# Optimization experiments

Hardware: AMD Instinct MI355X
Metric: run time of the kernel (lower is better)

Reference implementation:

```python
import jax, jax.numpy as jnp
import numpy as np
from jax.scipy.linalg import expm

B, S, D, E, K, NROT = 2, 2048, 1024, 8, 2, 3
EPS = 1e-5


def setup_inputs() -> dict:
    key = jax.random.key(0)
    ks = jax.random.split(key, 16)
    sc = 0.02
    x = jax.random.normal(ks[0], (B, S, D), jnp.float32)
    ln_gamma = 1.0 + sc * jax.random.normal(ks[1], (D,), jnp.float32)
    ln_beta = sc * jax.random.normal(ks[2], (D,), jnp.float32)
    abel_w = sc * jax.random.normal(ks[3], (D, D), jnp.float32)
    abel_b = sc * jax.random.normal(ks[4], (D,), jnp.float32)
    moe_gate_w = sc * jax.random.normal(ks[5], (D, E), jnp.float32)
    moe_gate_b = sc * jax.random.normal(ks[6], (E,), jnp.float32)
    ew1 = sc * jax.random.normal(ks[7], (E, D, 2 * D), jnp.float32)
    eb1 = sc * jax.random.normal(ks[8], (E, 2 * D), jnp.float32)
    ew2 = sc * jax.random.normal(ks[9], (E, 2 * D, D), jnp.float32)
    eb2 = sc * jax.random.normal(ks[10], (E, D), jnp.float32)
    g = sc * jax.random.normal(ks[11], (NROT, D, D), jnp.float32)
    gens = 0.5 * (g - jnp.swapaxes(g, -1, -2))  # skew-symmetric, as in reset_parameters
    gc_w = sc * jax.random.normal(ks[12], (2 * D, 1), jnp.float32)
    gc_b = sc * jax.random.normal(ks[13], (1,), jnp.float32)
    return dict(x=x, ln_gamma=ln_gamma, ln_beta=ln_beta, abel_w=abel_w, abel_b=abel_b,
                moe_gate_w=moe_gate_w, moe_gate_b=moe_gate_b, ew1=ew1, eb1=eb1,
                ew2=ew2, eb2=eb2, gens=gens, gc_w=gc_w, gc_b=gc_b)


def _gelu(x):
    return jax.nn.gelu(x, approximate=False)  # torch nn.GELU default = exact erf


def _forward(x, ln_gamma, ln_beta, abel_w, abel_b, moe_gate_w, moe_gate_b,
             ew1, eb1, ew2, eb2, gens, gc_w, gc_b):
    residual = x
    # LayerNorm
    mu = jnp.mean(x, axis=-1, keepdims=True)
    var = jnp.mean((x - mu) ** 2, axis=-1, keepdims=True)
    xn = (x - mu) * jax.lax.rsqrt(var + EPS) * ln_gamma + ln_beta
    # abel branch: Linear + GELU
    abel_out = _gelu(xn @ abel_w + abel_b)
    # MoE: dense all-experts compute, masked by top-k softmax weights
    logits = xn @ moe_gate_w + moe_gate_b                      # [B,S,E]
    topw, topi = jax.lax.top_k(logits, K)                      # [B,S,K]
    topw = jax.nn.softmax(topw, axis=-1)
    w_dense = jnp.sum(jax.nn.one_hot(topi, E, dtype=xn.dtype) * topw[..., None], axis=-2)  # [B,S,E]
    h = _gelu(jnp.einsum('bsd,edh->ebsh', xn, ew1) + eb1[:, None, None, :])  # [E,B,S,2D]
    eo = jnp.einsum('ebsh,ehd->ebsd', h, ew2) + eb2[:, None, None, :]        # [E,B,S,D]
    moe_out = jnp.einsum('ebsd,bse->bsd', eo, w_dense)
    # GeometricRotation: sequential matrix_exp rotations
    for i in range(NROT):
        moe_out = moe_out @ expm(gens[i])
    # gated residual mix
    combined = jnp.concatenate([abel_out, moe_out], axis=-1)
    gate = jax.nn.sigmoid(combined @ gc_w + gc_b)              # [B,S,1]
    mixed = abel_out * (1.0 - gate) + moe_out * gate
    return residual + mixed


def reference(x, ln_gamma, ln_beta, abel_w, abel_b, moe_gate_w, moe_gate_b,
              ew1, eb1, ew2, eb2, gens, gc_w, gc_b):
    return _forward(x, ln_gamma, ln_beta, abel_w, abel_b, moe_gate_w, moe_gate_b,
                    ew1, eb1, ew2, eb2, gens, gc_w, gc_b)
```

## Files before the change

### kernel.cpp

```cpp
#include <hip/hip_runtime.h>
#include <hip/hip_bf16.h>
#include <cstdint>
#include <cstddef>

#define DD   1024
#define DD2  2048
#define EE   8
#define NTOK 4096
#define CAPR 10240

typedef __bf16 bf16_t;
typedef __bf16 bf16x8 __attribute__((ext_vector_type(8)));
typedef __bf16 bf16x4 __attribute__((ext_vector_type(4)));
typedef float  f32x4v __attribute__((ext_vector_type(4)));

__device__ __forceinline__ float gelu_f(float v){
  const float t = v*(0.7978845608028654f + 0.0356774081f*v*v);
  const float u = __expf(2.0f*t);
  return __fdividef(v*u, 1.0f + u);
}

__device__ __forceinline__ void gload_lds16(const void* g, void* l){
  __builtin_amdgcn_global_load_lds(
    (const __attribute__((address_space(1))) unsigned int*)(uintptr_t)g,
    (__attribute__((address_space(3))) unsigned int*)(uintptr_t)l,
    16, 0, 0);
}

enum { EPI_GELU_F32=0, EPI_GELU_BF16=1, EPI_BIAS_BF16=2, EPI_SCALE_BF16=3,
       EPI_ADDV_BF16=4, EPI_BF16=5, EPI_F32=6 };

template<int BM,int BN,int EPI,bool DYN>
__global__ __launch_bounds__(256)
void gemm_bt(const bf16_t* __restrict__ A, const bf16_t* __restrict__ Bt,
             const int N, const int K, const int gx, const int gy, const int gz,
             const long sAz, const long sBz, const long sOz,
             const int* __restrict__ cnt, const int* __restrict__ offp,
             const float* __restrict__ bias, const long sBias,
             const float alpha,
             const bf16_t* __restrict__ addv,
             float* __restrict__ outF, bf16_t* __restrict__ outB)
{
  constexpr int BK = 64;
  constexpr int WM = BM/2, WN = BN/2;
  constexpr int FM = WM/16, FN = WN/16;
  constexpr int IA = BM/32, IB = BN/32;
  __shared__ alignas(16) bf16_t sA[2][BM*BK];
  __shared__ alignas(16) bf16_t sB[2][BN*BK];

  int bx, by, bz;
  if constexpr (DYN) {
    const int e = blockIdx.x & 7;
    const int i = blockIdx.x >> 3;
    bz = e; by = i / gx; bx = i - by*gx;
    if (by * BM >= cnt[e]) return;
  } else {
    const int nwg = gx * gy * gz;
    const int q = nwg >> 3, r = nwg & 7;
    const int k = blockIdx.x & 7, i = blockIdx.x >> 3;
    if (i >= q + (k < r ? 1 : 0)) return;
    const int l = k * q + (k < r ? k : r) + i;
    bx = l % gx; const int t2 = l / gx; by = t2 % gy; bz = t2 / gy;
  }

  const int z = bz;
  const bf16_t* Bp = Bt + (size_t)z * sBz;
  float*  oF = outF;
  bf16_t* oB = outB;
  if constexpr (DYN) {
    const long ro = offp[z];
    A  += ro * (long)K;
    oB += ro * (long)N;
  } else {
    A += (size_t)z * sAz;
    if (oF) oF += (size_t)z * sOz;
    if (oB) oB += (size_t)z * sOz;
  }
  const float*  bp = bias ? bias + (size_t)z * sBias : nullptr;
  const bf16_t* vp = addv ? addv + (size_t)z * sOz   : nullptr;

  const int tid = threadIdx.x;
  const int wid = tid >> 6, lid = tid & 63;
  const int wr = wid >> 1, wc = wid & 1;
  const int brow = by * BM, bcol = bx * BN;
  const int sr = lid >> 3, sq = lid & 7;
  const int fr = lid & 15, fq = lid >> 4;

  f32x4v acc[FM][FN] = {};

  auto stage = [&](int buf, int kt) {
    #pragma unroll
    for (int i = 0; i < IA; i++) {
      const int ii = wid*IA + i;
      const int r  = ii*8 + sr;
      const int q  = sq ^ (r & 7);
      gload_lds16((const char*)A + ((size_t)(brow + r)*K + kt)*2 + q*16,
                  (char*)sA[buf] + ii*1024);
    }
    #pragma unroll
    for (int i = 0; i < IB; i++) {
      const int ii = wid*IB + i;
      const int r  = ii*8 + sr;
      const int q  = sq ^ (r & 7);
      gload_lds16((const char*)Bp + ((size_t)(bcol + r)*K + kt)*2 + q*16,
                  (char*)sB[buf] + ii*1024);
    }
  };

  stage(0, 0);
  __syncthreads();
  int cur = 0;

  for (int kt = 0; kt < K; kt += BK) {
    if (kt + BK < K) stage(cur ^ 1, kt + BK);
    #pragma unroll
    for (int kk = 0; kk < 2; kk++) {
      bf16x8 af[FM], bb[FN];
      #pragma unroll
      for (int mi = 0; mi < FM; mi++) {
        const int r = wr*WM + mi*16 + fr;
        const int q = (kk*4 + fq) ^ (r & 7);
        af[mi] = *(const bf16x8*)((const char*)sA[cur] + r*128 + q*16);
      }
      #pragma unroll
      for (int ni = 0; ni < FN; ni++) {
        const int r = wc*WN + ni*16 + fr;
        const int q = (kk*4 + fq) ^ (r & 7);
        bb[ni] = *(const bf16x8*)((const char*)sB[cur] + r*128 + q*16);
      }
      #pragma unroll
      for (int mi = 0; mi < FM; mi++)
        #pragma unroll
        for (int ni = 0; ni < FN; ni++)
          acc[mi][ni] = __builtin_amdgcn_mfma_f32_16x16x32_bf16(
              af[mi], bb[ni], acc[mi][ni], 0, 0, 0);
    }
    __syncthreads();
    cur ^= 1;
  }

  #pragma unroll
  for (int mi = 0; mi < FM; mi++) {
    #pragma unroll
    for (int ni = 0; ni < FN; ni++) {
      const int rg0 = brow + wr*WM + mi*16 + fq*4;
      const int cg  = bcol + wc*WN + ni*16 + fr;
      #pragma unroll
      for (int i = 0; i < 4; i++) {
        const int rg = rg0 + i;
        float v = acc[mi][ni][i];
        if constexpr (EPI == EPI_GELU_F32) {
          v += bp[cg];
          oF[(size_t)rg*N + cg] = gelu_f(v);
        } else if constexpr (EPI == EPI_GELU_BF16) {
          v += bp[cg];
          oB[(size_t)rg*N + cg] = (bf16_t)gelu_f(v);
        } else if constexpr (EPI == EPI_BIAS_BF16) {
          v += bp[cg];
          oB[(size_t)rg*N + cg] = (bf16_t)v;
        } else if constexpr (EPI == EPI_SCALE_BF16) {
          oB[(size_t)rg*N + cg] = (bf16_t)(v * alpha);
        } else if constexpr (EPI == EPI_ADDV_BF16) {
          oB[(size_t)rg*N + cg] = (bf16_t)(v + (float)vp[(size_t)rg*N + cg]);
        } else if constexpr (EPI == EPI_BF16) {
          oB[(size_t)rg*N + cg] = (bf16_t)v;
        } else {
          oF[(size_t)rg*N + cg] = v;
        }
      }
    }
  }
}

__global__ __launch_bounds__(256)
void tcvt_kernel(const float* __restrict__ src, bf16_t* __restrict__ dst, int R, int C){
  __shared__ float tile[32][33];
  const size_t bo = (size_t)blockIdx.z * R * C;
  const int c0 = blockIdx.x*32, r0 = blockIdx.y*32;
  #pragma unroll
  for (int i = 0; i < 4; i++) {
    const int r = r0 + threadIdx.y + i*8;
    tile[threadIdx.y + i*8][threadIdx.x] = src[bo + (size_t)r*C + c0 + threadIdx.x];
  }
  __syncthreads();
  #pragma unroll
  for (int i = 0; i < 4; i++) {
    const int c = c0 + threadIdx.y + i*8;
    dst[bo + (size_t)c*R + r0 + threadIdx.x] = (bf16_t)tile[threadIdx.x][threadIdx.y + i*8];
  }
}

__global__ __launch_bounds__(256)
void tb16_kernel(const bf16_t* __restrict__ Ut, bf16_t* __restrict__ Tb){
  __shared__ bf16_t tile[32][33];
  const bf16_t* src = Ut + (size_t)(1 - blockIdx.z) * DD * DD;
  bf16_t*       dst = Tb + (size_t)blockIdx.z * DD * DD;
  const int c0 = blockIdx.x*32, r0 = blockIdx.y*32;
  #pragma unroll
  for (int i = 0; i < 4; i++)
    tile[threadIdx.y + i*8][threadIdx.x] = src[(size_t)(r0 + threadIdx.y + i*8)*DD + c0 + threadIdx.x];
  __syncthreads();
  #pragma unroll
  for (int i = 0; i < 4; i++)
    dst[(size_t)(c0 + threadIdx.y + i*8)*DD + r0 + threadIdx.x] = tile[threadIdx.x][threadIdx.y + i*8];
}

__global__ __launch_bounds__(256)
void cvt_kernel(const float* __restrict__ in, bf16_t* __restrict__ o, long n, float scale){
  const long i = ((long)blockIdx.x*256 + threadIdx.x)*4;
  if (i >= n) return;
  const float4 v = *(const float4*)(in + i);
  bf16x4 b; b[0]=(bf16_t)(v.x*scale); b[1]=(bf16_t)(v.y*scale);
  b[2]=(bf16_t)(v.z*scale); b[3]=(bf16_t)(v.w*scale);
  *(bf16x4*)(o + i) = b;
}

__global__ __launch_bounds__(256)
void vw_kernel(const bf16_t* __restrict__ Hn, const bf16_t* __restrict__ H2,
               bf16_t* __restrict__ Vb, bf16_t* __restrict__ Wtb){
  const long i0 = ((long)blockIdx.x*256 + threadIdx.x)*4;
  const long rc = i0 % (long)(DD*DD);
  const int r = (int)(rc / DD), c0 = (int)(rc % DD);
  const bf16x4 h  = *(const bf16x4*)(Hn + i0);
  const bf16x4 h2 = *(const bf16x4*)(H2 + i0);
  bf16x4 v, w;
  #pragma unroll
  for (int j = 0; j < 4; j++) {
    const float d  = (r == c0 + j) ? 1.0f : 0.0f;
    const float fh = (float)h[j], f2 = (float)h2[j];
    v[j] = (bf16_t)(d + fh + f2*0.5f);
    w[j] = (bf16_t)(d*(1.0f/6.0f) - fh*(1.0f/24.0f) + f2*(1.0f/120.0f));
  }
  *(bf16x4*)(Vb  + i0) = v;
  *(bf16x4*)(Wtb + i0) = w;
}

__global__ __launch_bounds__(256)
void ln_gate_kernel(const float* __restrict__ x, const float* __restrict__ gamma,
                    const float* __restrict__ beta, const float* __restrict__ gw,
                    const float* __restrict__ gb,
                    bf16_t* __restrict__ xnb, int2* __restrict__ ids,
                    float2* __restrict__ wts)
{
  const int t = blockIdx.x, tid = threadIdx.x, j0 = tid*4;
  const int wid = tid >> 6, lid = tid & 63;
  const float4 v = *(const float4*)(x + (size_t)t*DD + j0);
  float s  = v.x + v.y + v.z + v.w;
  float ss = v.x*v.x + v.y*v.y + v.z*v.z + v.w*v.w;
  #pragma unroll
  for (int off = 32; off; off >>= 1) { s += __shfl_down(s, off); ss += __shfl_down(ss, off); }
  __shared__ float redS[4], redQ[4], mv[2];
  if (lid == 0) { redS[wid] = s; redQ[wid] = ss; }
  __syncthreads();
  if (tid == 0) {
    const float S1 = redS[0]+redS[1]+redS[2]+redS[3];
    const float S2 = redQ[0]+redQ[1]+redQ[2]+redQ[3];
    const float mu  = S1 * (1.0f/DD);
    const float var = S2 * (1.0f/DD) - mu*mu;
    mv[0] = mu; mv[1] = rsqrtf(var + 1e-5f);
  }
  __syncthreads();
  const float mu = mv[0], rstd = mv[1];
  const float4 g = *(const float4*)(gamma + j0);
  const float4 b = *(const float4*)(beta  + j0);
  float xn[4];
  xn[0] = (v.x-mu)*rstd*g.x + b.x;
  xn[1] = (v.y-mu)*rstd*g.y + b.y;
  xn[2] = (v.z-mu)*rstd*g.z + b.z;
  xn[3] = (v.w-mu)*rstd*g.w + b.w;
  bf16x4 ov; ov[0]=(bf16_t)xn[0]; ov[1]=(bf16_t)xn[1]; ov[2]=(bf16_t)xn[2]; ov[3]=(bf16_t)xn[3];
  *(bf16x4*)(xnb + (size_t)t*DD + j0) = ov;

  float p[8] = {0,0,0,0,0,0,0,0};
  #pragma unroll
  for (int i = 0; i < 4; i++) {
    const float4 a0 = *(const float4*)(gw + (size_t)(j0+i)*EE);
    const float4 a1 = *(const float4*)(gw + (size_t)(j0+i)*EE + 4);
    const float xv = xn[i];
    p[0]+=xv*a0.x; p[1]+=xv*a0.y; p[2]+=xv*a0.z; p[3]+=xv*a0.w;
    p[4]+=xv*a1.x; p[5]+=xv*a1.y; p[6]+=xv*a1.z; p[7]+=xv*a1.w;
  }
  #pragma unroll
  for (int off = 32; off; off >>= 1) {
    #pragma unroll
    for (int e = 0; e < 8; e++) p[e] += __shfl_down(p[e], off);
  }
  __shared__ float pr[32];
  if (lid == 0) {
    #pragma unroll
    for (int e = 0; e < 8; e++) pr[wid*8 + e] = p[e];
  }
  __syncthreads();
  if (tid == 0) {
    float l[8];
    #pragma unroll
    for (int e = 0; e < 8; e++) l[e] = pr[e] + pr[8+e] + pr[16+e] + pr[24+e] + gb[e];
    int i1 = 0; float m1 = l[0];
    #pragma unroll
    for (int e = 1; e < 8; e++) if (l[e] > m1) { m1 = l[e]; i1 = e; }
    int i2 = 0; float m2 = -1e30f;
    #pragma unroll
    for (int e = 0; e < 8; e++) if (e != i1 && l[e] > m2) { m2 = l[e]; i2 = e; }
    const float wa = 1.0f/(1.0f + expf(m2 - m1));
    ids[t] = make_int2(i1, i2);
    wts[t] = make_float2(wa, 1.0f - wa);
  }
}

__global__ __launch_bounds__(256)
void route_kernel(const int2* __restrict__ ids, int* __restrict__ slotA,
                  int* __restrict__ slotB, int* __restrict__ cnt,
                  int* __restrict__ off)
{
  const int tid = threadIdx.x;
  const int wid = tid >> 6, lid = tid & 63;
  __shared__ int wsum[EE][4];
  __shared__ int base[EE];
  if (tid < EE) base[tid] = 0;
  __syncthreads();
  const unsigned long long lt = (1ull << lid) - 1ull;
  for (int c0 = 0; c0 < NTOK; c0 += 256) {
    const int t = c0 + tid;
    const int2 id = ids[t];
    int pA = 0, pB = 0;
    #pragma unroll
    for (int e = 0; e < EE; e++) {
      const bool fA = (id.x == e), fB = (id.y == e);
      const unsigned long long mA = __ballot(fA);
      const unsigned long long mB = __ballot(fB);
      const int cA = __popcll(mA);
      if (lid == 0) wsum[e][wid] = cA + __popcll(mB);
      if (fA) pA = __popcll(mA & lt);
      if (fB) pB = cA + __popcll(mB & lt);
    }
    __syncthreads();
    int wbA = base[id.x], wbB = base[id.y];
    for (int w = 0; w < wid; w++) { wbA += wsum[id.x][w]; wbB += wsum[id.y][w]; }
    slotA[t] = wbA + pA;
    slotB[t] = wbB + pB;
    __syncthreads();
    if (tid < EE) base[tid] += wsum[tid][0]+wsum[tid][1]+wsum[tid][2]+wsum[tid][3];
    __syncthreads();
  }
  if (tid == 0) {
    int a = 0;
    #pragma unroll
    for (int e = 0; e < EE; e++) { cnt[e] = base[e]; off[e] = a; a += (base[e]+255)&~255; }
  }
}

__global__ __launch_bounds__(256)
void gather_kernel(const bf16_t* __restrict__ xnb, const int2* __restrict__ ids,
                   const int* __restrict__ slotA, const int* __restrict__ slotB,
                   const int* __restrict__ off, bf16_t* __restrict__ Xg){
  const int t = blockIdx.x, j = threadIdx.x*4;
  const int2 id = ids[t];
  const bf16x4 v = *(const bf16x4*)(xnb + (size_t)t*DD + j);
  *(bf16x4*)(Xg + (size_t)(off[id.x] + slotA[t])*DD + j) = v;
  *(bf16x4*)(Xg + (size_t)(off[id.y] + slotB[t])*DD + j) = v;
}

__global__ __launch_bounds__(256)
void combine_kernel(const bf16_t* __restrict__ Yg, const int2* __restrict__ ids,
                    const int* __restrict__ slotA, const int* __restrict__ slotB,
                    const int* __restrict__ off, const float2* __restrict__ wts,
                    bf16_t* __restrict__ Xa){
  const int t = blockIdx.x, j = threadIdx.x*4;
  const int2 id = ids[t];
  const float2 w = wts[t];
  const bf16x4 a = *(const bf16x4*)(Yg + (size_t)(off[id.x] + slotA[t])*DD + j);
  const bf16x4 b = *(const bf16x4*)(Yg + (size_t)(off[id.y] + slotB[t])*DD + j);
  bf16x4 o;
  #pragma unroll
  for (int i = 0; i < 4; i++) o[i] = (bf16_t)(w.x*(float)a[i] + w.y*(float)b[i]);
  *(bf16x4*)(Xa + (size_t)t*DD + j) = o;
}

__global__ __launch_bounds__(256)
void mix_kernel(const float* __restrict__ x, const bf16_t* __restrict__ abel,
                const float* __restrict__ rot, const float* __restrict__ gcw,
                const float* __restrict__ gcb, float* __restrict__ out)
{
  const int t = blockIdx.x, tid = threadIdx.x, j0 = tid*4;
  const int wid = tid >> 6, lid = tid & 63;
  const bf16x4 ab = *(const bf16x4*)(abel + (size_t)t*DD + j0);
  const float4 r  = *(const float4*)(rot  + (size_t)t*DD + j0);
  const float4 ga = *(const float4*)(gcw + j0);
  const float4 gr = *(const float4*)(gcw + DD + j0);
  const float a0 = (float)ab[0], a1 = (float)ab[1], a2 = (float)ab[2], a3 = (float)ab[3];
  float p = a0*ga.x + a1*ga.y + a2*ga.z + a3*ga.w
          + r.x*gr.x + r.y*gr.y + r.z*gr.z + r.w*gr.w;
  #pragma unroll
  for (int off = 32; off; off >>= 1) p += __shfl_down(p, off);
  __shared__ float red[4];
  __shared__ float gsh;
  if (lid == 0) red[wid] = p;
  __syncthreads();
  if (tid == 0) {
    const float P = red[0] + red[1] + red[2] + red[3] + gcb[0];
    gsh = 1.0f/(1.0f + expf(-P));
  }
  __syncthreads();
  const float gate = gsh, g1 = 1.0f - gate;
  const float4 xv = *(const float4*)(x + (size_t)t*DD + j0);
  float4 o;
  o.x = xv.x + a0*g1 + r.x*gate;
  o.y = xv.y + a1*g1 + r.y*gate;
  o.z = xv.z + a2*g1 + r.z*gate;
  o.w = xv.w + a3*g1 + r.w*gate;
  *(float4*)(out + (size_t)t*DD + j0) = o;
}

extern "C" void kernel_launch(void* const* d_in, const int* in_sizes, int n_in,
                              void* d_out, int out_size, void* d_ws, size_t ws_size,
                              hipStream_t stream)
{
  (void)in_sizes; (void)n_in; (void)out_size; (void)ws_size;
  const float* x      = (const float*)d_in[0];
  const float* ln_g   = (const float*)d_in[1];
  const float* ln_b   = (const float*)d_in[2];
  const float* abel_w = (const float*)d_in[3];
  const float* abel_b = (const float*)d_in[4];
  const float* gate_w = (const float*)d_in[5];
  const float* gate_b = (const float*)d_in[6];
  const float* ew1    = (const float*)d_in[7];
  const float* eb1    = (const float*)d_in[8];
  const float* ew2    = (const float*)d_in[9];
  const float* eb2    = (const float*)d_in[10];
  const float* gens   = (const float*)d_in[11];
  const float* gc_w   = (const float*)d_in[12];
  const float* gc_b   = (const float*)d_in[13];
  float* out = (float*)d_out;

  char* wsp = (char*)d_ws;
  auto alloc = [&](size_t bytes) -> char* {
    char* p = wsp; wsp += (bytes + 255) & ~(size_t)255; return p;
  };
  const size_t MB = 1u<<20;
  bf16_t* xnb   = (bf16_t*)alloc((size_t)NTOK*DD*2);
  int2*   ids   = (int2*)  alloc((size_t)NTOK*8);
  float2* wts   = (float2*)alloc((size_t)NTOK*8);
  int*    slotA = (int*)   alloc((size_t)NTOK*4);
  int*    slotB = (int*)   alloc((size_t)NTOK*4);
  int*    cnt   = (int*)   alloc(64);
  int*    off   = (int*)   alloc(64);
  bf16_t* abel_wT = (bf16_t*)alloc((size_t)DD*DD*2);
  char*   UN      = alloc(64*MB);
  bf16_t* ew1T  = (bf16_t*)UN;
  bf16_t* ew2T  = (bf16_t*)(UN + 32*MB);
  bf16_t* Hn    = (bf16_t*)alloc((size_t)3*DD*DD*2);
  bf16_t* abelo = (bf16_t*)alloc((size_t)NTOK*DD*2);
  bf16_t* Xg    = (bf16_t*)alloc((size_t)CAPR*DD*2);
  bf16_t* Hg    = (bf16_t*)alloc((size_t)CAPR*DD2*2);
  bf16_t* Xa    = (bf16_t*)alloc((size_t)NTOK*DD*2);
  bf16_t* Yg    = Xg;
  float*  rot   = (float*)Hg;
  bf16_t* H2  = (bf16_t*)(UN + 0*MB);
  bf16_t* H3  = (bf16_t*)(UN + 6*MB);
  bf16_t* Vb  = (bf16_t*)(UN + 12*MB);
  bf16_t* Wtb = (bf16_t*)(UN + 18*MB);
  bf16_t* Ut  = (bf16_t*)(UN + 24*MB);
  bf16_t* Tb  = (bf16_t*)(UN + 30*MB);
  bf16_t* Pb  = (bf16_t*)(UN + 34*MB);
  bf16_t* Rt  = (bf16_t*)(UN + 36*MB);
  const long D2 = (long)DD*DD;

  auto gflat = [](int gx, int gy, int gz) {
    const int nwg = gx*gy*gz; return 8 * ((nwg + 7) / 8);
  };

  const dim3 tb(32, 8, 1);
  tcvt_kernel<<<dim3(DD/32,  DD/32, 1),  tb, 0, stream>>>(abel_w, abel_wT, DD,  DD);
  tcvt_kernel<<<dim3(DD2/32, DD/32, EE), tb, 0, stream>>>(ew1,    ew1T,    DD,  DD2);
  tcvt_kernel<<<dim3(DD/32,  DD2/32,EE), tb, 0, stream>>>(ew2,    ew2T,    DD2, DD);
  cvt_kernel<<<dim3(3*DD*DD/1024,1,1), 256, 0, stream>>>(gens, Hn, (long)3*DD*DD, -1.0f);

  ln_gate_kernel<<<dim3(NTOK,1,1), 256, 0, stream>>>(x, ln_g, ln_b, gate_w, gate_b,
                                                     xnb, ids, wts);
  route_kernel<<<dim3(1,1,1), 256, 0, stream>>>(ids, slotA, slotB, cnt, off);
  gather_kernel<<<dim3(NTOK,1,1), 256, 0, stream>>>(xnb, ids, slotA, slotB, off, Xg);

  gemm_bt<128,128,EPI_GELU_BF16,true><<<dim3(8*(DD2/128)*(NTOK/128),1,1), 256, 0, stream>>>(
      Xg, ew1T, DD2, DD, DD2/128, NTOK/128, EE, 0, (long)DD2*DD, 0,
      cnt, off, eb1, DD2, 1.0f, nullptr, nullptr, Hg);
  gemm_bt<128,128,EPI_BIAS_BF16,true><<<dim3(8*(DD/128)*(NTOK/128),1,1), 256, 0, stream>>>(
      Hg, ew2T, DD, DD2, DD/128, NTOK/128, EE, 0, (long)DD*DD2, 0,
      cnt, off, eb2, DD, 1.0f, nullptr, nullptr, Yg);
  combine_kernel<<<dim3(NTOK,1,1), 256, 0, stream>>>(Yg, ids, slotA, slotB, off, wts, Xa);

  gemm_bt<128,64,EPI_GELU_BF16,false><<<dim3(gflat(16,32,1),1,1), 256, 0, stream>>>(
      xnb, abel_wT, DD, DD, 16, 32, 1, 0, 0, 0, nullptr, nullptr,
      abel_b, 0, 1.0f, nullptr, nullptr, abelo);

  gemm_bt<128,64,EPI_SCALE_BF16,false><<<dim3(gflat(16,8,3),1,1), 256, 0, stream>>>(
      Hn, Hn, DD, DD, 16, 8, 3, D2, D2, D2, nullptr, nullptr,
      nullptr, 0, -1.0f, nullptr, nullptr, H2);
  gemm_bt<128,64,EPI_SCALE_BF16,false><<<dim3(gflat(16,8,3),1,1), 256, 0, stream>>>(
      H2, Hn, DD, DD, 16, 8, 3, D2, D2, D2, nullptr, nullptr,
      nullptr, 0, -1.0f, nullptr, nullptr, H3);
  vw_kernel<<<dim3(3*DD*DD/1024,1,1), 256, 0, stream>>>(Hn, H2, Vb, Wtb);
  gemm_bt<128,64,EPI_ADDV_BF16,false><<<dim3(gflat(16,8,3),1,1), 256, 0, stream>>>(
      H3, Wtb, DD, DD, 16, 8, 3, D2, D2, D2, nullptr, nullptr,
      nullptr, 0, 1.0f, Vb, nullptr, Ut);
  tb16_kernel<<<dim3(32,32,2), tb, 0, stream>>>(Ut, Tb);
  gemm_bt<64,64,EPI_BF16,false><<<dim3(gflat(16,16,1),1,1), 256, 0, stream>>>(
      Ut + 2*D2, Tb, DD, DD, 16, 16, 1, 0, 0, 0, nullptr, nullptr,
      nullptr, 0, 1.0f, nullptr, nullptr, Pb);
  gemm_bt<64,64,EPI_BF16,false><<<dim3(gflat(16,16,1),1,1), 256, 0, stream>>>(
      Pb, Tb + D2, DD, DD, 16, 16, 1, 0, 0, 0, nullptr, nullptr,
      nullptr, 0, 1.0f, nullptr, nullptr, Rt);
  gemm_bt<128,64,EPI_F32,false><<<dim3(gflat(16,32,1),1,1), 256, 0, stream>>>(
      Xa, Rt, DD, DD, 16, 32, 1, 0, 0, 0, nullptr, nullptr,
      nullptr, 0, 1.0f, nullptr, rot, nullptr);

  mix_kernel<<<dim3(NTOK,1,1), 256, 0, stream>>>(x, abelo, rot, gc_w, gc_b, out);
}
```

Measured before the change: 347.9 us.

## Schedule MoE expert GEMMs via compact tile table and vectorize weight transposes

The route kernel now builds a compact list of (expert, row-offset) 128-row tiles and pads each expert only to 128 rows instead of 256. The grouped expert GEMMs launch over at most this tile table with XCD-aware block remapping, so they no longer launch and early-exit a dense grid sized for every expert at full token count. The fp32-to-bf16 weight transpose kernels also move to 64x64 tiles with float4 loads and bf16x4 stores to cut memory transactions. The tile table is built serially by one thread, and a MAXT cap of 72 tiles is assumed to bound the worst case.

```diff
diff --git a/kernel.cpp b/kernel.cpp
--- a/kernel.cpp
+++ b/kernel.cpp
@@ -7,7 +7,8 @@
 #define DD2  2048
 #define EE   8
 #define NTOK 4096
-#define CAPR 10240
+#define CAPR 9216
+#define MAXT 72
 
 typedef __bf16 bf16_t;
 typedef __bf16 bf16x8 __attribute__((ext_vector_type(8)));
@@ -30,12 +31,13 @@
 enum { EPI_GELU_F32=0, EPI_GELU_BF16=1, EPI_BIAS_BF16=2, EPI_SCALE_BF16=3,
        EPI_ADDV_BF16=4, EPI_BF16=5, EPI_F32=6 };
 
-template<int BM,int BN,int EPI,bool DYN>
+template<int BM,int BN,int EPI,bool TAB>
 __global__ __launch_bounds__(256)
 void gemm_bt(const bf16_t* __restrict__ A, const bf16_t* __restrict__ Bt,
              const int N, const int K, const int gx, const int gy, const int gz,
              const long sAz, const long sBz, const long sOz,
-             const int* __restrict__ cnt, const int* __restrict__ offp,
+             const int* __restrict__ tileE, const int* __restrict__ tileR,
+             const int* __restrict__ ntp, const int* __restrict__ offp,
              const float* __restrict__ bias, const long sBias,
              const float alpha,
              const bf16_t* __restrict__ addv,
@@ -49,11 +51,19 @@
   __shared__ alignas(16) bf16_t sB[2][BN*BK];
 
   int bx, by, bz;
-  if constexpr (DYN) {
-    const int e = blockIdx.x & 7;
-    const int i = blockIdx.x >> 3;
-    bz = e; by = i / gx; bx = i - by*gx;
-    if (by * BM >= cnt[e]) return;
+  if constexpr (TAB) {
+    const int nwg = gx * gy;
+    const int q = nwg >> 3, r = nwg & 7;
+    const int k = blockIdx.x & 7, i = blockIdx.x >> 3;
+    if (i >= q + (k < r ? 1 : 0)) return;
+    const int l = k * q + (k < r ? k : r) + i;
+    const int ti = l / gx; bx = l - ti*gx;
+    if (ti >= ntp[0]) return;
+    bz = tileE[ti];
+    by = 0;
+    const long ro = (long)offp[bz] + tileR[ti];
+    A    += ro * (long)K;
+    outB += ro * (long)N;
   } else {
     const int nwg = gx * gy * gz;
     const int q = nwg >> 3, r = nwg & 7;
@@ -67,11 +77,7 @@
   const bf16_t* Bp = Bt + (size_t)z * sBz;
   float*  oF = outF;
   bf16_t* oB = outB;
-  if constexpr (DYN) {
-    const long ro = offp[z];
-    A  += ro * (long)K;
-    oB += ro * (long)N;
-  } else {
+  if constexpr (!TAB) {
     A += (size_t)z * sAz;
     if (oF) oF += (size_t)z * sOz;
     if (oB) oB += (size_t)z * sOz;
@@ -174,19 +180,25 @@
 
 __global__ __launch_bounds__(256)
 void tcvt_kernel(const float* __restrict__ src, bf16_t* __restrict__ dst, int R, int C){
-  __shared__ float tile[32][33];
+  __shared__ float t[64][65];
   const size_t bo = (size_t)blockIdx.z * R * C;
-  const int c0 = blockIdx.x*32, r0 = blockIdx.y*32;
+  const int c0 = blockIdx.x*64, r0 = blockIdx.y*64;
+  const int lx = threadIdx.x & 15, ly = threadIdx.x >> 4;
   #pragma unroll
   for (int i = 0; i < 4; i++) {
-    const int r = r0 + threadIdx.y + i*8;
-    tile[threadIdx.y + i*8][threadIdx.x] = src[bo + (size_t)r*C + c0 + threadIdx.x];
+    const int row = r0 + ly + i*16;
+    const float4 v = *(const float4*)(src + bo + (size_t)row*C + c0 + lx*4);
+    t[ly + i*16][lx*4+0] = v.x; t[ly + i*16][lx*4+1] = v.y;
+    t[ly + i*16][lx*4+2] = v.z; t[ly + i*16][lx*4+3] = v.w;
   }
   __syncthreads();
   #pragma unroll
   for (int i = 0; i < 4; i++) {
-    const int c = c0 + threadIdx.y + i*8;
-    dst[bo + (size_t)c*R + r0 + threadIdx.x] = (bf16_t)tile[threadIdx.x][threadIdx.y + i*8];
+    const int c = c0 + ly + i*16;
+    bf16x4 o;
+    #pragma unroll
+    for (int j = 0; j < 4; j++) o[j] = (bf16_t)t[lx*4+j][ly + i*16];
+    *(bf16x4*)(dst + bo + (size_t)c*R + r0 + lx*4) = o;
   }
 }
 
@@ -310,7 +322,8 @@
 __global__ __launch_bounds__(256)
 void route_kernel(const int2* __restrict__ ids, int* __restrict__ slotA,
                   int* __restrict__ slotB, int* __restrict__ cnt,
-                  int* __restrict__ off)
+                  int* __restrict__ off, int* __restrict__ tileE,
+                  int* __restrict__ tileR, int* __restrict__ ntp)
 {
   const int tid = threadIdx.x;
   const int wid = tid >> 6, lid = tid & 63;
@@ -343,9 +356,13 @@
     __syncthreads();
   }
   if (tid == 0) {
-    int a = 0;
-    #pragma unroll
-    for (int e = 0; e < EE; e++) { cnt[e] = base[e]; off[e] = a; a += (base[e]+255)&~255; }
+    int a = 0, nt = 0;
+    for (int e = 0; e < EE; e++) {
+      cnt[e] = base[e]; off[e] = a;
+      for (int r2 = 0; r2 < base[e]; r2 += 128) { tileE[nt] = e; tileR[nt] = r2; nt++; }
+      a += (base[e] + 127) & ~127;
+    }
+    ntp[0] = nt;
   }
 }
 
@@ -444,6 +461,9 @@
   int*    slotB = (int*)   alloc((size_t)NTOK*4);
   int*    cnt   = (int*)   alloc(64);
   int*    off   = (int*)   alloc(64);
+  int*    tileE = (int*)   alloc(MAXT*4);
+  int*    tileR = (int*)   alloc(MAXT*4);
+  int*    ntp   = (int*)   alloc(64);
   bf16_t* abel_wT = (bf16_t*)alloc((size_t)DD*DD*2);
   char*   UN      = alloc(64*MB);
   bf16_t* ew1T  = (bf16_t*)UN;
@@ -469,48 +489,48 @@
     const int nwg = gx*gy*gz; return 8 * ((nwg + 7) / 8);
   };
 
-  const dim3 tb(32, 8, 1);
-  tcvt_kernel<<<dim3(DD/32,  DD/32, 1),  tb, 0, stream>>>(abel_w, abel_wT, DD,  DD);
-  tcvt_kernel<<<dim3(DD2/32, DD/32, EE), tb, 0, stream>>>(ew1,    ew1T,    DD,  DD2);
-  tcvt_kernel<<<dim3(DD/32,  DD2/32,EE), tb, 0, stream>>>(ew2,    ew2T,    DD2, DD);
+  tcvt_kernel<<<dim3(DD/64,  DD/64, 1),  256, 0, stream>>>(abel_w, abel_wT, DD,  DD);
+  tcvt_kernel<<<dim3(DD2/64, DD/64, EE), 256, 0, stream>>>(ew1,    ew1T,    DD,  DD2);
+  tcvt_kernel<<<dim3(DD/64,  DD2/64,EE), 256, 0, stream>>>(ew2,    ew2T,    DD2, DD);
   cvt_kernel<<<dim3(3*DD*DD/1024,1,1), 256, 0, stream>>>(gens, Hn, (long)3*DD*DD, -1.0f);
 
   ln_gate_kernel<<<dim3(NTOK,1,1), 256, 0, stream>>>(x, ln_g, ln_b, gate_w, gate_b,
                                                      xnb, ids, wts);
-  route_kernel<<<dim3(1,1,1), 256, 0, stream>>>(ids, slotA, slotB, cnt, off);
+  route_kernel<<<dim3(1,1,1), 256, 0, stream>>>(ids, slotA, slotB, cnt, off,
+                                                tileE, tileR, ntp);
   gather_kernel<<<dim3(NTOK,1,1), 256, 0, stream>>>(xnb, ids, slotA, slotB, off, Xg);
 
-  gemm_bt<128,128,EPI_GELU_BF16,true><<<dim3(8*(DD2/128)*(NTOK/128),1,1), 256, 0, stream>>>(
-      Xg, ew1T, DD2, DD, DD2/128, NTOK/128, EE, 0, (long)DD2*DD, 0,
-      cnt, off, eb1, DD2, 1.0f, nullptr, nullptr, Hg);
-  gemm_bt<128,128,EPI_BIAS_BF16,true><<<dim3(8*(DD/128)*(NTOK/128),1,1), 256, 0, stream>>>(
-      Hg, ew2T, DD, DD2, DD/128, NTOK/128, EE, 0, (long)DD*DD2, 0,
-      cnt, off, eb2, DD, 1.0f, nullptr, nullptr, Yg);
+  gemm_bt<128,128,EPI_GELU_BF16,true><<<dim3((DD2/128)*MAXT,1,1), 256, 0, stream>>>(
+      Xg, ew1T, DD2, DD, DD2/128, MAXT, 1, 0, (long)DD2*DD, 0,
+      tileE, tileR, ntp, off, eb1, DD2, 1.0f, nullptr, nullptr, Hg);
+  gemm_bt<128,128,EPI_BIAS_BF16,true><<<dim3((DD/128)*MAXT,1,1), 256, 0, stream>>>(
+      Hg, ew2T, DD, DD2, DD/128, MAXT, 1, 0, (long)DD*DD2, 0,
+      tileE, tileR, ntp, off, eb2, DD, 1.0f, nullptr, nullptr, Yg);
   combine_kernel<<<dim3(NTOK,1,1), 256, 0, stream>>>(Yg, ids, slotA, slotB, off, wts, Xa);
 
   gemm_bt<128,64,EPI_GELU_BF16,false><<<dim3(gflat(16,32,1),1,1), 256, 0, stream>>>(
-      xnb, abel_wT, DD, DD, 16, 32, 1, 0, 0, 0, nullptr, nullptr,
+      xnb, abel_wT, DD, DD, 16, 32, 1, 0, 0, 0, nullptr, nullptr, nullptr, nullptr,
       abel_b, 0, 1.0f, nullptr, nullptr, abelo);
 
   gemm_bt<128,64,EPI_SCALE_BF16,false><<<dim3(gflat(16,8,3),1,1), 256, 0, stream>>>(
-      Hn, Hn, DD, DD, 16, 8, 3, D2, D2, D2, nullptr, nullptr,
+      Hn, Hn, DD, DD, 16, 8, 3, D2, D2, D2, nullptr, nullptr, nullptr, nullptr,
       nullptr, 0, -1.0f, nullptr, nullptr, H2);
   gemm_bt<128,64,EPI_SCALE_BF16,false><<<dim3(gflat(16,8,3),1,1), 256, 0, stream>>>(
-      H2, Hn, DD, DD, 16, 8, 3, D2, D2, D2, nullptr, nullptr,
+      H2, Hn, DD, DD, 16, 8, 3, D2, D2, D2, nullptr, nullptr, nullptr, nullptr,
       nullptr, 0, -1.0f, nullptr, nullptr, H3);
   vw_kernel<<<dim3(3*DD*DD/1024,1,1), 256, 0, stream>>>(Hn, H2, Vb, Wtb);
   gemm_bt<128,64,EPI_ADDV_BF16,false><<<dim3(gflat(16,8,3),1,1), 256, 0, stream>>>(
-      H3, Wtb, DD, DD, 16, 8, 3, D2, D2, D2, nullptr, nullptr,
+      H3, Wtb, DD, DD, 16, 8, 3, D2, D2, D2, nullptr, nullptr, nullptr, nullptr,
       nullptr, 0, 1.0f, Vb, nullptr, Ut);
-  tb16_kernel<<<dim3(32,32,2), tb, 0, stream>>>(Ut, Tb);
+  tb16_kernel<<<dim3(32,32,2), dim3(32,8,1), 0, stream>>>(Ut, Tb);
   gemm_bt<64,64,EPI_BF16,false><<<dim3(gflat(16,16,1),1,1), 256, 0, stream>>>(
-      Ut + 2*D2, Tb, DD, DD, 16, 16, 1, 0, 0, 0, nullptr, nullptr,
+      Ut + 2*D2, Tb, DD, DD, 16, 16, 1, 0, 0, 0, nullptr, nullptr, nullptr, nullptr,
       nullptr, 0, 1.0f, nullptr, nullptr, Pb);
   gemm_bt<64,64,EPI_BF16,false><<<dim3(gflat(16,16,1),1,1), 256, 0, stream>>>(
-      Pb, Tb + D2, DD, DD, 16, 16, 1, 0, 0, 0, nullptr, nullptr,
+      Pb, Tb + D2, DD, DD, 16, 16, 1, 0, 0, 0, nullptr, nullptr, nullptr, nullptr,
       nullptr, 0, 1.0f, nullptr, nullptr, Rt);
   gemm_bt<128,64,EPI_F32,false><<<dim3(gflat(16,32,1),1,1), 256, 0, stream>>>(
-      Xa, Rt, DD, DD, 16, 32, 1, 0, 0, 0, nullptr, nullptr,
+      Xa, Rt, DD, DD, 16, 32, 1, 0, 0, 0, nullptr, nullptr, nullptr, nullptr,
       nullptr, 0, 1.0f, nullptr, rot, nullptr);
 
   mix_kernel<<<dim3(NTOK,1,1), 256, 0, stream>>>(x, abelo, rot, gc_w, gc_b, out);
```

Result: no change. 342.8 us (-1.5%).
